# Kernel optimization log

Measured on AMD Instinct MI355X. Metric: run time of the kernel, lower is better.

## Reference

```python
import jax, jax.numpy as jnp
import numpy as np

B, S, H, NH, SLOTS, SD = 4, 2048, 1024, 16, 16, 32
HD = H // NH  # head_dim = 64


def setup_inputs() -> dict:
    key = jax.random.key(0)
    ks = jax.random.split(key, 8)
    def w(k, shape, scale=0.02):
        return jax.random.normal(k, shape, jnp.float32) * scale
    return {
        "hidden_states": jax.random.normal(ks[0], (B, S, H), jnp.float32),
        "stack": jax.random.normal(ks[1], (B, S, NH, SLOTS, SD), jnp.float32),
        "mask": jnp.ones((B, S, NH, SLOTS), jnp.float32),
        "Wa": w(ks[2], (H, 3 * NH)), "ba": jnp.zeros((3 * NH,), jnp.float32),
        "Wd": w(ks[3], (HD, SD)), "bd": jnp.zeros((SD,), jnp.float32),
        "Wu": w(ks[4], (SD, HD)), "bu": jnp.zeros((HD,), jnp.float32),
        "Wg": w(ks[5], (SD, 1)), "bg": jnp.zeros((1,), jnp.float32),
        "res_weight": jnp.ones((1,), jnp.float32),
    }


def reference(hidden_states, stack, mask, Wa, ba, Wd, bd, Wu, bu, Wg, bg, res_weight):
    b, s, h = hidden_states.shape
    # action logits, scaled by sqrt(head_dim), softmax over {push,pop,noop}
    logits = (hidden_states @ Wa + ba) / jnp.sqrt(jnp.float32(HD))
    actions = jax.nn.softmax(logits.reshape(b, s, NH, 3), axis=-1)  # [B,S,NH,3]
    # per-head key values projected down to stack_dim
    k = hidden_states.reshape(b, s, NH, HD) @ Wd + bd  # [B,S,NH,SD]
    # soft push / pop / noop stack update (fused weighted sum; no [.,3,.] stack tensor)
    push_stack = jnp.concatenate([k[..., None, :], stack[..., :-1, :]], axis=3)
    pop_stack = jnp.concatenate([stack[..., 1:, :], jnp.zeros_like(stack[..., :1, :])], axis=3)
    push_mask = jnp.concatenate([jnp.ones_like(mask[..., :1]), mask[..., :-1]], axis=3)
    pop_mask = jnp.concatenate([mask[..., 1:], jnp.zeros_like(mask[..., :1])], axis=3)
    a_push = actions[..., 0]
    a_pop = actions[..., 1]
    a_noop = actions[..., 2]
    new_stack = (a_push[..., None, None] * push_stack
                 + a_pop[..., None, None] * pop_stack
                 + a_noop[..., None, None] * stack)  # [B,S,NH,SLOTS,SD]
    new_mask = (a_push[..., None] * push_mask
                + a_pop[..., None] * pop_mask
                + a_noop[..., None] * mask)  # [B,S,NH,SLOTS]
    # gated readout over stack slots
    gate_scores = (new_stack @ Wg)[..., 0] + bg[0]  # [B,S,NH,SLOTS]
    gate = jax.nn.softmax(gate_scores + (1.0 - new_mask) * -1e9, axis=-1)
    mem = jnp.sum(new_stack * gate[..., None], axis=3)  # [B,S,NH,SD]
    mem = mem @ Wu + bu  # [B,S,NH,HD]
    out = mem.reshape(b, s, h) * res_weight[0] + hidden_states
    return (out, new_stack, new_mask)
```

## Files before the change

### kernel.cpp

```cpp
#include <hip/hip_runtime.h>


constexpr long long OUT_STACK_OFF = 8388608LL;
constexpr long long OUT_MASK_OFF  = 75497472LL;

__global__ void transpose_wa(const float* __restrict__ Wa, float* __restrict__ WaT) {
    int o = blockIdx.x * 256 + threadIdx.x;
    if (o < 48 * 1024) {
        int j = o >> 10, i = o & 1023;
        WaT[o] = Wa[i * 48 + j];
    }
}

__device__ __forceinline__ float dot4(float4 a, float4 b) {
    return a.x * b.x + a.y * b.y + a.z * b.z + a.w * b.w;
}

__device__ __forceinline__ float4 shfl4(float4 v, int src) {
    return make_float4(__shfl(v.x, src), __shfl(v.y, src),
                       __shfl(v.z, src), __shfl(v.w, src));
}

__device__ __forceinline__ float4 sel4(bool c, float4 a, float4 b) {
    return make_float4(c ? a.x : b.x, c ? a.y : b.y, c ? a.z : b.z, c ? a.w : b.w);
}

__global__ __launch_bounds__(256)
void proj_kernel(const float* __restrict__ hid,
                 const float* __restrict__ WaT,
                 const float* __restrict__ ba,
                 const float* __restrict__ Wd,
                 const float* __restrict__ bd,
                 float* __restrict__ out)
{
    const int t = threadIdx.x;
    const int wv = t >> 6, lane = t & 63;
    const int tok0 = blockIdx.x * 4;
    float* stash = out + OUT_STACK_OFF;
    const float4* hid4 = (const float4*)hid + (size_t)tok0 * 256;

    float4 hreg[4][4];
    #pragma unroll
    for (int tt = 0; tt < 4; ++tt)
        #pragma unroll
        for (int m = 0; m < 4; ++m)
            hreg[tt][m] = hid4[tt * 256 + m * 64 + lane];

    const float4* waT4 = (const float4*)WaT;
    #pragma unroll
    for (int jj = 0; jj < 12; ++jj) {
        int j = wv * 12 + jj;
        float a0 = 0.f, a1 = 0.f, a2 = 0.f, a3 = 0.f;
        #pragma unroll
        for (int m = 0; m < 4; ++m) {
            float4 w = waT4[j * 256 + m * 64 + lane];
            a0 += dot4(hreg[0][m], w);
            a1 += dot4(hreg[1][m], w);
            a2 += dot4(hreg[2][m], w);
            a3 += dot4(hreg[3][m], w);
        }
        #pragma unroll
        for (int off = 1; off <= 32; off <<= 1) {
            a0 += __shfl_xor(a0, off);
            a1 += __shfl_xor(a1, off);
            a2 += __shfl_xor(a2, off);
            a3 += __shfl_xor(a3, off);
        }
        if ((lane & 15) == jj) {
            int tt = lane >> 4;
            float v = (tt == 0) ? a0 : (tt == 1) ? a1 : (tt == 2) ? a2 : a3;
            int nh = wv * 4 + jj / 3, a = jj - 3 * (jj / 3);
            stash[(size_t)(tok0 + tt) * 8192 + nh * 512 + 32 + a] = (v + ba[j]) * 0.125f;
        }
    }

    const int d = t & 31, nhg = t >> 5;
    float acc0[4], acc1[4];
    float bdv = bd[d];
    #pragma unroll
    for (int tt = 0; tt < 4; ++tt) { acc0[tt] = bdv; acc1[tt] = bdv; }
    #pragma unroll
    for (int ii = 0; ii < 16; ++ii) {
        float w0 = Wd[(4 * ii + 0) * 32 + d];
        float w1 = Wd[(4 * ii + 1) * 32 + d];
        float w2 = Wd[(4 * ii + 2) * 32 + d];
        float w3 = Wd[(4 * ii + 3) * 32 + d];
        #pragma unroll
        for (int tt = 0; tt < 4; ++tt) {
            float4 ha = hid4[tt * 256 + nhg * 16 + ii];
            float4 hb = hid4[tt * 256 + (nhg + 8) * 16 + ii];
            acc0[tt] += ha.x * w0 + ha.y * w1 + ha.z * w2 + ha.w * w3;
            acc1[tt] += hb.x * w0 + hb.y * w1 + hb.z * w2 + hb.w * w3;
        }
    }
    #pragma unroll
    for (int tt = 0; tt < 4; ++tt) {
        stash[(size_t)(tok0 + tt) * 8192 + nhg * 512 + d] = acc0[tt];
        stash[(size_t)(tok0 + tt) * 8192 + (nhg + 8) * 512 + d] = acc1[tt];
    }
}

__global__ __launch_bounds__(256, 4)
void stack_main(const float* __restrict__ stack,
                const float* __restrict__ mask,
                const float* __restrict__ hid,
                const float* __restrict__ Wg,
                const float* __restrict__ bgp,
                const float* __restrict__ Wu,
                const float* __restrict__ bu,
                const float* __restrict__ resw,
                float* __restrict__ out)
{
    __shared__ __align__(16) float sh_mem[4][32];
    const int t = threadIdx.x, wv = t >> 6, l = t & 63;
    const int wid = blockIdx.x * 4 + wv;
    const int tok = wid >> 4, nh = wid & 15;

    const float4* stk4 = (const float4*)stack + (size_t)tok * 2048 + nh * 128;
    float* ostack = out + OUT_STACK_OFF + (size_t)tok * 8192 + nh * 512;
    const float4* stash4 = (const float4*)ostack;

    float4 A  = stk4[l];
    float4 Bv = stk4[64 + l];
    float4 kv = stash4[l & 7];
    float4 lg = stash4[8];
    const float* mrow_g = mask + (size_t)tok * 256 + nh * 16;
    float mA = mrow_g[l >> 3];
    float mB = mrow_g[8 + (l >> 3)];
    float4 wg = *(const float4*)(Wg + (l & 7) * 4);

    float mx = fmaxf(lg.x, fmaxf(lg.y, lg.z));
    float e0 = __expf(lg.x - mx), e1 = __expf(lg.y - mx), e2 = __expf(lg.z - mx);
    float ainv = 1.f / (e0 + e1 + e2);
    float ap = e0 * ainv, apop = e1 * ainv, an = e2 * ainv;

    float4 Am  = shfl4(A,  l - 8);
    float4 Apl = shfl4(A,  l + 8);
    float4 BfA = shfl4(A,  l + 56);
    float4 AfB = shfl4(Bv, l - 56);
    float4 Bm  = shfl4(Bv, l - 8);
    float4 Bp  = shfl4(Bv, l + 8);
    float sAm = __shfl(mA, l - 8), sAp = __shfl(mA, l + 8), sA56 = __shfl(mA, l + 56);
    float sBm = __shfl(mB, l - 8), sBp = __shfl(mB, l + 8), sB56 = __shfl(mB, l - 56);

    const bool lo = (l < 8), hi = (l >= 56);
    float4 prevA = sel4(lo, kv, Am);
    float4 nextA = sel4(hi, AfB, Apl);
    float4 prevB = sel4(lo, BfA, Bm);
    float4 nextB = sel4(hi, make_float4(0.f, 0.f, 0.f, 0.f), Bp);
    float pmA = lo ? 1.f : sAm;
    float nmA = hi ? sB56 : sAp;
    float pmB = lo ? sA56 : sBm;
    float nmB = hi ? 0.f : sBp;

    float4 nA, nB;
    nA.x = ap * prevA.x + apop * nextA.x + an * A.x;
    nA.y = ap * prevA.y + apop * nextA.y + an * A.y;
    nA.z = ap * prevA.z + apop * nextA.z + an * A.z;
    nA.w = ap * prevA.w + apop * nextA.w + an * A.w;
    nB.x = ap * prevB.x + apop * nextB.x + an * Bv.x;
    nB.y = ap * prevB.y + apop * nextB.y + an * Bv.y;
    nB.z = ap * prevB.z + apop * nextB.z + an * Bv.z;
    nB.w = ap * prevB.w + apop * nextB.w + an * Bv.w;
    float nmaskA = ap * pmA + apop * nmA + an * mA;
    float nmaskB = ap * pmB + apop * nmB + an * mB;

    float4* ost4 = (float4*)ostack;
    ost4[l] = nA;
    ost4[64 + l] = nB;
    if ((l & 7) == 0) {
        float* om = out + OUT_MASK_OFF + (size_t)tok * 256 + nh * 16;
        om[l >> 3] = nmaskA;
        om[8 + (l >> 3)] = nmaskB;
    }

    float gA = dot4(nA, wg);
    float gB = dot4(nB, wg);
    #pragma unroll
    for (int off = 1; off <= 4; off <<= 1) {
        gA += __shfl_xor(gA, off);
        gB += __shfl_xor(gB, off);
    }
    float bgv = bgp[0];
    gA += bgv + (1.f - nmaskA) * -1e9f;
    gB += bgv + (1.f - nmaskB) * -1e9f;

    float gm = fmaxf(gA, gB);
    #pragma unroll
    for (int off = 8; off <= 32; off <<= 1) gm = fmaxf(gm, __shfl_xor(gm, off));
    float eA = __expf(gA - gm), eB = __expf(gB - gm);
    float es = eA + eB;
    #pragma unroll
    for (int off = 8; off <= 32; off <<= 1) es += __shfl_xor(es, off);
    float ginv = 1.f / es;
    float gateA = eA * ginv, gateB = eB * ginv;

    float4 sv;
    sv.x = gateA * nA.x + gateB * nB.x;
    sv.y = gateA * nA.y + gateB * nB.y;
    sv.z = gateA * nA.z + gateB * nB.z;
    sv.w = gateA * nA.w + gateB * nB.w;
    #pragma unroll
    for (int off = 8; off <= 32; off <<= 1) {
        sv.x += __shfl_xor(sv.x, off);
        sv.y += __shfl_xor(sv.y, off);
        sv.z += __shfl_xor(sv.z, off);
        sv.w += __shfl_xor(sv.w, off);
    }
    if (l < 8) *(float4*)&sh_mem[wv][l * 4] = sv;
    __syncthreads();

    float acc = bu[l];
    const float* mrow = sh_mem[wv];
    #pragma unroll
    for (int dd = 0; dd < 32; ++dd)
        acc += mrow[dd] * Wu[dd * 64 + l];
    size_t oidx = (size_t)tok * 1024 + nh * 64 + l;
    out[oidx] = acc * resw[0] + hid[oidx];
}

extern "C" void kernel_launch(void* const* d_in, const int* in_sizes, int n_in,
                              void* d_out, int out_size, void* d_ws, size_t ws_size,
                              hipStream_t stream) {
    const float* hid  = (const float*)d_in[0];
    const float* stk  = (const float*)d_in[1];
    const float* msk  = (const float*)d_in[2];
    const float* Wa   = (const float*)d_in[3];
    const float* ba   = (const float*)d_in[4];
    const float* Wd   = (const float*)d_in[5];
    const float* bd   = (const float*)d_in[6];
    const float* Wu   = (const float*)d_in[7];
    const float* bu   = (const float*)d_in[8];
    const float* Wg   = (const float*)d_in[9];
    const float* bg   = (const float*)d_in[10];
    const float* rw   = (const float*)d_in[11];
    float* out = (float*)d_out;
    float* waT = (float*)d_ws;

    transpose_wa<<<192, 256, 0, stream>>>(Wa, waT);
    proj_kernel<<<2048, 256, 0, stream>>>(hid, waT, ba, Wd, bd, out);
    stack_main<<<32768, 256, 0, stream>>>(stk, msk, hid, Wg, bg, Wu, bu, rw, out);
}
```

Before: 596.7 us.

## Fuse action and key projections into the stack kernel, dropping the stash round-trip

Removes the separate projection kernel and computes the action logits and the down-projected key inside the stack kernel. Each block stages one token's hidden row in shared memory. This avoids writing and re-reading a stash in the output buffer and saves a launch. It also remaps block indices with a swizzle, and the Wu readout now uses shuffles instead of a shared-memory round trip. The cost is that each token's hidden row is loaded by four blocks, and the logit and Wd dot products are now computed per head by each wave instead of being amortised across four tokens.

```diff
diff --git a/kernel.cpp b/kernel.cpp
--- a/kernel.cpp
+++ b/kernel.cpp
@@ -25,85 +25,14 @@
     return make_float4(c ? a.x : b.x, c ? a.y : b.y, c ? a.z : b.z, c ? a.w : b.w);
 }
 
-__global__ __launch_bounds__(256)
-void proj_kernel(const float* __restrict__ hid,
-                 const float* __restrict__ WaT,
-                 const float* __restrict__ ba,
-                 const float* __restrict__ Wd,
-                 const float* __restrict__ bd,
-                 float* __restrict__ out)
-{
-    const int t = threadIdx.x;
-    const int wv = t >> 6, lane = t & 63;
-    const int tok0 = blockIdx.x * 4;
-    float* stash = out + OUT_STACK_OFF;
-    const float4* hid4 = (const float4*)hid + (size_t)tok0 * 256;
-
-    float4 hreg[4][4];
-    #pragma unroll
-    for (int tt = 0; tt < 4; ++tt)
-        #pragma unroll
-        for (int m = 0; m < 4; ++m)
-            hreg[tt][m] = hid4[tt * 256 + m * 64 + lane];
-
-    const float4* waT4 = (const float4*)WaT;
-    #pragma unroll
-    for (int jj = 0; jj < 12; ++jj) {
-        int j = wv * 12 + jj;
-        float a0 = 0.f, a1 = 0.f, a2 = 0.f, a3 = 0.f;
-        #pragma unroll
-        for (int m = 0; m < 4; ++m) {
-            float4 w = waT4[j * 256 + m * 64 + lane];
-            a0 += dot4(hreg[0][m], w);
-            a1 += dot4(hreg[1][m], w);
-            a2 += dot4(hreg[2][m], w);
-            a3 += dot4(hreg[3][m], w);
-        }
-        #pragma unroll
-        for (int off = 1; off <= 32; off <<= 1) {
-            a0 += __shfl_xor(a0, off);
-            a1 += __shfl_xor(a1, off);
-            a2 += __shfl_xor(a2, off);
-            a3 += __shfl_xor(a3, off);
-        }
-        if ((lane & 15) == jj) {
-            int tt = lane >> 4;
-            float v = (tt == 0) ? a0 : (tt == 1) ? a1 : (tt == 2) ? a2 : a3;
-            int nh = wv * 4 + jj / 3, a = jj - 3 * (jj / 3);
-            stash[(size_t)(tok0 + tt) * 8192 + nh * 512 + 32 + a] = (v + ba[j]) * 0.125f;
-        }
-    }
-
-    const int d = t & 31, nhg = t >> 5;
-    float acc0[4], acc1[4];
-    float bdv = bd[d];
-    #pragma unroll
-    for (int tt = 0; tt < 4; ++tt) { acc0[tt] = bdv; acc1[tt] = bdv; }
-    #pragma unroll
-    for (int ii = 0; ii < 16; ++ii) {
-        float w0 = Wd[(4 * ii + 0) * 32 + d];
-        float w1 = Wd[(4 * ii + 1) * 32 + d];
-        float w2 = Wd[(4 * ii + 2) * 32 + d];
-        float w3 = Wd[(4 * ii + 3) * 32 + d];
-        #pragma unroll
-        for (int tt = 0; tt < 4; ++tt) {
-            float4 ha = hid4[tt * 256 + nhg * 16 + ii];
-            float4 hb = hid4[tt * 256 + (nhg + 8) * 16 + ii];
-            acc0[tt] += ha.x * w0 + ha.y * w1 + ha.z * w2 + ha.w * w3;
-            acc1[tt] += hb.x * w0 + hb.y * w1 + hb.z * w2 + hb.w * w3;
-        }
-    }
-    #pragma unroll
-    for (int tt = 0; tt < 4; ++tt) {
-        stash[(size_t)(tok0 + tt) * 8192 + nhg * 512 + d] = acc0[tt];
-        stash[(size_t)(tok0 + tt) * 8192 + (nhg + 8) * 512 + d] = acc1[tt];
-    }
-}
-
 __global__ __launch_bounds__(256, 4)
-void stack_main(const float* __restrict__ stack,
+void stack_main(const float* __restrict__ hid,
+                const float* __restrict__ stack,
                 const float* __restrict__ mask,
-                const float* __restrict__ hid,
+                const float* __restrict__ WaT,
+                const float* __restrict__ ba,
+                const float* __restrict__ Wd,
+                const float* __restrict__ bd,
                 const float* __restrict__ Wg,
                 const float* __restrict__ bgp,
                 const float* __restrict__ Wu,
@@ -111,28 +40,60 @@
                 const float* __restrict__ resw,
                 float* __restrict__ out)
 {
-    __shared__ __align__(16) float sh_mem[4][32];
+    __shared__ __align__(16) float sh_hid[1024];
+
     const int t = threadIdx.x, wv = t >> 6, l = t & 63;
-    const int wid = blockIdx.x * 4 + wv;
-    const int tok = wid >> 4, nh = wid & 15;
+    const int raw = blockIdx.x;
+    const int sb  = (raw >> 3) + ((raw & 7) << 12);
+    const int tok = sb >> 2;
+    const int nh  = ((sb & 3) << 2) + wv;
+
+    const float4* hid4g = (const float4*)(hid + (size_t)tok * 1024);
+    ((float4*)sh_hid)[t] = hid4g[t];
+    __syncthreads();
+
+    float4 hreg[4];
+    #pragma unroll
+    for (int m = 0; m < 4; ++m) hreg[m] = ((const float4*)sh_hid)[m * 64 + l];
+    const float4* waT4 = (const float4*)WaT;
+    float lac[3];
+    #pragma unroll
+    for (int a = 0; a < 3; ++a) {
+        int j = nh * 3 + a;
+        float acc = 0.f;
+        #pragma unroll
+        for (int m = 0; m < 4; ++m)
+            acc += dot4(hreg[m], waT4[j * 256 + m * 64 + l]);
+        #pragma unroll
+        for (int off = 1; off <= 32; off <<= 1) acc += __shfl_xor(acc, off);
+        lac[a] = (acc + ba[j]) * 0.125f;
+    }
+    float mx = fmaxf(lac[0], fmaxf(lac[1], lac[2]));
+    float e0 = __expf(lac[0] - mx), e1 = __expf(lac[1] - mx), e2 = __expf(lac[2] - mx);
+    float ainv = 1.f / (e0 + e1 + e2);
+    float ap = e0 * ainv, apop = e1 * ainv, an = e2 * ainv;
+
+    const int d = l & 31, hh = l >> 5;
+    const float* hrow = sh_hid + nh * 64 + hh * 32;
+    float kacc = 0.f;
+    #pragma unroll
+    for (int i = 0; i < 32; ++i)
+        kacc += hrow[i] * Wd[(hh * 32 + i) * 32 + d];
+    kacc += __shfl_xor(kacc, 32);
+    kacc += bd[d];
+    float4 kv;
+    kv.x = __shfl(kacc, ((l & 7) << 2) + 0);
+    kv.y = __shfl(kacc, ((l & 7) << 2) + 1);
+    kv.z = __shfl(kacc, ((l & 7) << 2) + 2);
+    kv.w = __shfl(kacc, ((l & 7) << 2) + 3);
 
     const float4* stk4 = (const float4*)stack + (size_t)tok * 2048 + nh * 128;
-    float* ostack = out + OUT_STACK_OFF + (size_t)tok * 8192 + nh * 512;
-    const float4* stash4 = (const float4*)ostack;
-
     float4 A  = stk4[l];
     float4 Bv = stk4[64 + l];
-    float4 kv = stash4[l & 7];
-    float4 lg = stash4[8];
     const float* mrow_g = mask + (size_t)tok * 256 + nh * 16;
     float mA = mrow_g[l >> 3];
     float mB = mrow_g[8 + (l >> 3)];
     float4 wg = *(const float4*)(Wg + (l & 7) * 4);
-
-    float mx = fmaxf(lg.x, fmaxf(lg.y, lg.z));
-    float e0 = __expf(lg.x - mx), e1 = __expf(lg.y - mx), e2 = __expf(lg.z - mx);
-    float ainv = 1.f / (e0 + e1 + e2);
-    float ap = e0 * ainv, apop = e1 * ainv, an = e2 * ainv;
 
     float4 Am  = shfl4(A,  l - 8);
     float4 Apl = shfl4(A,  l + 8);
@@ -165,6 +126,7 @@
     float nmaskA = ap * pmA + apop * nmA + an * mA;
     float nmaskB = ap * pmB + apop * nmB + an * mB;
 
+    float* ostack = out + OUT_STACK_OFF + (size_t)tok * 8192 + nh * 512;
     float4* ost4 = (float4*)ostack;
     ost4[l] = nA;
     ost4[64 + l] = nB;
@@ -207,16 +169,18 @@
         sv.z += __shfl_xor(sv.z, off);
         sv.w += __shfl_xor(sv.w, off);
     }
-    if (l < 8) *(float4*)&sh_mem[wv][l * 4] = sv;
-    __syncthreads();
 
     float acc = bu[l];
-    const float* mrow = sh_mem[wv];
-    #pragma unroll
-    for (int dd = 0; dd < 32; ++dd)
-        acc += mrow[dd] * Wu[dd * 64 + l];
+    #pragma unroll
+    for (int q = 0; q < 8; ++q) {
+        float4 mq = shfl4(sv, q);
+        acc += mq.x * Wu[(q * 4 + 0) * 64 + l]
+             + mq.y * Wu[(q * 4 + 1) * 64 + l]
+             + mq.z * Wu[(q * 4 + 2) * 64 + l]
+             + mq.w * Wu[(q * 4 + 3) * 64 + l];
+    }
     size_t oidx = (size_t)tok * 1024 + nh * 64 + l;
-    out[oidx] = acc * resw[0] + hid[oidx];
+    out[oidx] = acc * resw[0] + sh_hid[nh * 64 + l];
 }
 
 extern "C" void kernel_launch(void* const* d_in, const int* in_sizes, int n_in,
@@ -238,6 +202,6 @@
     float* waT = (float*)d_ws;
 
     transpose_wa<<<192, 256, 0, stream>>>(Wa, waT);
-    proj_kernel<<<2048, 256, 0, stream>>>(hid, waT, ba, Wd, bd, out);
-    stack_main<<<32768, 256, 0, stream>>>(stk, msk, hid, Wg, bg, Wu, bu, rw, out);
-}
+    stack_main<<<32768, 256, 0, stream>>>(hid, stk, msk, waT, ba, Wd, bd,
+                                          Wg, bg, Wu, bu, rw, out);
+}
```

Result: slower. 653.0 us (+9.4%).

## Process two heads per wave in stack kernel and use permlane32 swap reductions

Applied to the files above, without the earlier changes.

The stack update kernel now handles two heads per wavefront, which halves the grid and issues the loads for both heads up front so more memory traffic is in flight per wave. The cross-half reduction step (xor 32) in both kernels is replaced with the permlane32_swap builtin when available, avoiding a DPP-unfriendly shuffle. The Wu readout reads the shared memory row as float4. The cost is higher register pressure per thread, which can lower occupancy in a kernel that is mostly bandwidth-bound.

```diff
diff --git a/kernel.cpp b/kernel.cpp
--- a/kernel.cpp
+++ b/kernel.cpp
@@ -24,6 +24,23 @@
 __device__ __forceinline__ float4 sel4(bool c, float4 a, float4 b) {
     return make_float4(c ? a.x : b.x, c ? a.y : b.y, c ? a.z : b.z, c ? a.w : b.w);
 }
+
+#if defined(__has_builtin) && __has_builtin(__builtin_amdgcn_permlane32_swap)
+typedef int v2i_t __attribute__((ext_vector_type(2)));
+__device__ __forceinline__ float red32_add(float x) {
+    v2i_t r = __builtin_amdgcn_permlane32_swap(__float_as_int(x), __float_as_int(x),
+                                               false, false);
+    return __int_as_float(r.x) + __int_as_float(r.y);
+}
+__device__ __forceinline__ float red32_max(float x) {
+    v2i_t r = __builtin_amdgcn_permlane32_swap(__float_as_int(x), __float_as_int(x),
+                                               false, false);
+    return fmaxf(__int_as_float(r.x), __int_as_float(r.y));
+}
+#else
+__device__ __forceinline__ float red32_add(float x) { return x + __shfl_xor(x, 32); }
+__device__ __forceinline__ float red32_max(float x) { return fmaxf(x, __shfl_xor(x, 32)); }
+#endif
 
 __global__ __launch_bounds__(256)
 void proj_kernel(const float* __restrict__ hid,
@@ -60,12 +77,13 @@
             a3 += dot4(hreg[3][m], w);
         }
         #pragma unroll
-        for (int off = 1; off <= 32; off <<= 1) {
+        for (int off = 1; off <= 16; off <<= 1) {
             a0 += __shfl_xor(a0, off);
             a1 += __shfl_xor(a1, off);
             a2 += __shfl_xor(a2, off);
             a3 += __shfl_xor(a3, off);
         }
+        a0 = red32_add(a0); a1 = red32_add(a1); a2 = red32_add(a2); a3 = red32_add(a3);
         if ((lane & 15) == jj) {
             int tt = lane >> 4;
             float v = (tt == 0) ? a0 : (tt == 1) ? a1 : (tt == 2) ? a2 : a3;
@@ -111,112 +129,149 @@
                 const float* __restrict__ resw,
                 float* __restrict__ out)
 {
-    __shared__ __align__(16) float sh_mem[4][32];
+    __shared__ __align__(16) float sh_mem[4][2][32];
     const int t = threadIdx.x, wv = t >> 6, l = t & 63;
-    const int wid = blockIdx.x * 4 + wv;
-    const int tok = wid >> 4, nh = wid & 15;
-
-    const float4* stk4 = (const float4*)stack + (size_t)tok * 2048 + nh * 128;
-    float* ostack = out + OUT_STACK_OFF + (size_t)tok * 8192 + nh * 512;
-    const float4* stash4 = (const float4*)ostack;
-
-    float4 A  = stk4[l];
-    float4 Bv = stk4[64 + l];
-    float4 kv = stash4[l & 7];
-    float4 lg = stash4[8];
-    const float* mrow_g = mask + (size_t)tok * 256 + nh * 16;
-    float mA = mrow_g[l >> 3];
-    float mB = mrow_g[8 + (l >> 3)];
-    float4 wg = *(const float4*)(Wg + (l & 7) * 4);
-
-    float mx = fmaxf(lg.x, fmaxf(lg.y, lg.z));
-    float e0 = __expf(lg.x - mx), e1 = __expf(lg.y - mx), e2 = __expf(lg.z - mx);
-    float ainv = 1.f / (e0 + e1 + e2);
-    float ap = e0 * ainv, apop = e1 * ainv, an = e2 * ainv;
-
-    float4 Am  = shfl4(A,  l - 8);
-    float4 Apl = shfl4(A,  l + 8);
-    float4 BfA = shfl4(A,  l + 56);
-    float4 AfB = shfl4(Bv, l - 56);
-    float4 Bm  = shfl4(Bv, l - 8);
-    float4 Bp  = shfl4(Bv, l + 8);
-    float sAm = __shfl(mA, l - 8), sAp = __shfl(mA, l + 8), sA56 = __shfl(mA, l + 56);
-    float sBm = __shfl(mB, l - 8), sBp = __shfl(mB, l + 8), sB56 = __shfl(mB, l - 56);
-
+    const int bid = blockIdx.x;
+    const int tok = bid >> 1;
+    const int nhb = ((bid & 1) << 3) + wv;
+
+    const float4* stkt = (const float4*)stack + (size_t)tok * 2048;
+    float* ostack_base = out + OUT_STACK_OFF + (size_t)tok * 8192;
+    const float* mrow_g = mask + (size_t)tok * 256;
+
+    float4 A[2], Bv[2], kv[2], lgv[2];
+    float mA[2], mB[2];
+    #pragma unroll
+    for (int u = 0; u < 2; ++u) {
+        const int nh = nhb + 4 * u;
+        const float4* stk4 = stkt + nh * 128;
+        A[u]  = stk4[l];
+        Bv[u] = stk4[64 + l];
+        const float4* stash4 = (const float4*)(ostack_base + nh * 512);
+        kv[u]  = stash4[l & 7];
+        lgv[u] = stash4[8];
+        mA[u] = mrow_g[nh * 16 + (l >> 3)];
+        mB[u] = mrow_g[nh * 16 + 8 + (l >> 3)];
+    }
+    const float4 wg = *(const float4*)(Wg + (l & 7) * 4);
+    const float bgv = bgp[0];
     const bool lo = (l < 8), hi = (l >= 56);
-    float4 prevA = sel4(lo, kv, Am);
-    float4 nextA = sel4(hi, AfB, Apl);
-    float4 prevB = sel4(lo, BfA, Bm);
-    float4 nextB = sel4(hi, make_float4(0.f, 0.f, 0.f, 0.f), Bp);
-    float pmA = lo ? 1.f : sAm;
-    float nmA = hi ? sB56 : sAp;
-    float pmB = lo ? sA56 : sBm;
-    float nmB = hi ? 0.f : sBp;
-
-    float4 nA, nB;
-    nA.x = ap * prevA.x + apop * nextA.x + an * A.x;
-    nA.y = ap * prevA.y + apop * nextA.y + an * A.y;
-    nA.z = ap * prevA.z + apop * nextA.z + an * A.z;
-    nA.w = ap * prevA.w + apop * nextA.w + an * A.w;
-    nB.x = ap * prevB.x + apop * nextB.x + an * Bv.x;
-    nB.y = ap * prevB.y + apop * nextB.y + an * Bv.y;
-    nB.z = ap * prevB.z + apop * nextB.z + an * Bv.z;
-    nB.w = ap * prevB.w + apop * nextB.w + an * Bv.w;
-    float nmaskA = ap * pmA + apop * nmA + an * mA;
-    float nmaskB = ap * pmB + apop * nmB + an * mB;
-
-    float4* ost4 = (float4*)ostack;
-    ost4[l] = nA;
-    ost4[64 + l] = nB;
-    if ((l & 7) == 0) {
-        float* om = out + OUT_MASK_OFF + (size_t)tok * 256 + nh * 16;
-        om[l >> 3] = nmaskA;
-        om[8 + (l >> 3)] = nmaskB;
-    }
-
-    float gA = dot4(nA, wg);
-    float gB = dot4(nB, wg);
-    #pragma unroll
-    for (int off = 1; off <= 4; off <<= 1) {
-        gA += __shfl_xor(gA, off);
-        gB += __shfl_xor(gB, off);
-    }
-    float bgv = bgp[0];
-    gA += bgv + (1.f - nmaskA) * -1e9f;
-    gB += bgv + (1.f - nmaskB) * -1e9f;
-
-    float gm = fmaxf(gA, gB);
-    #pragma unroll
-    for (int off = 8; off <= 32; off <<= 1) gm = fmaxf(gm, __shfl_xor(gm, off));
-    float eA = __expf(gA - gm), eB = __expf(gB - gm);
-    float es = eA + eB;
-    #pragma unroll
-    for (int off = 8; off <= 32; off <<= 1) es += __shfl_xor(es, off);
-    float ginv = 1.f / es;
-    float gateA = eA * ginv, gateB = eB * ginv;
-
-    float4 sv;
-    sv.x = gateA * nA.x + gateB * nB.x;
-    sv.y = gateA * nA.y + gateB * nB.y;
-    sv.z = gateA * nA.z + gateB * nB.z;
-    sv.w = gateA * nA.w + gateB * nB.w;
-    #pragma unroll
-    for (int off = 8; off <= 32; off <<= 1) {
-        sv.x += __shfl_xor(sv.x, off);
-        sv.y += __shfl_xor(sv.y, off);
-        sv.z += __shfl_xor(sv.z, off);
-        sv.w += __shfl_xor(sv.w, off);
-    }
-    if (l < 8) *(float4*)&sh_mem[wv][l * 4] = sv;
+
+    float ap[2], apop[2], an[2];
+    #pragma unroll
+    for (int u = 0; u < 2; ++u) {
+        float mx = fmaxf(lgv[u].x, fmaxf(lgv[u].y, lgv[u].z));
+        float e0 = __expf(lgv[u].x - mx), e1 = __expf(lgv[u].y - mx), e2 = __expf(lgv[u].z - mx);
+        float ainv = 1.f / (e0 + e1 + e2);
+        ap[u] = e0 * ainv; apop[u] = e1 * ainv; an[u] = e2 * ainv;
+    }
+
+    float4 nA[2], nB[2];
+    float nmaskA[2], nmaskB[2];
+    #pragma unroll
+    for (int u = 0; u < 2; ++u) {
+        float4 Am  = shfl4(A[u],  l - 8);
+        float4 Apl = shfl4(A[u],  l + 8);
+        float4 BfA = shfl4(A[u],  l + 56);
+        float4 AfB = shfl4(Bv[u], l - 56);
+        float4 Bm  = shfl4(Bv[u], l - 8);
+        float4 Bp  = shfl4(Bv[u], l + 8);
+        float sAm = __shfl(mA[u], l - 8), sAp = __shfl(mA[u], l + 8), sA56 = __shfl(mA[u], l + 56);
+        float sBm = __shfl(mB[u], l - 8), sBp = __shfl(mB[u], l + 8), sB56 = __shfl(mB[u], l - 56);
+
+        float4 prevA = sel4(lo, kv[u], Am);
+        float4 nextA = sel4(hi, AfB, Apl);
+        float4 prevB = sel4(lo, BfA, Bm);
+        float4 nextB = sel4(hi, make_float4(0.f, 0.f, 0.f, 0.f), Bp);
+        float pmA = lo ? 1.f : sAm;
+        float nmA = hi ? sB56 : sAp;
+        float pmB = lo ? sA56 : sBm;
+        float nmB = hi ? 0.f : sBp;
+
+        nA[u].x = ap[u] * prevA.x + apop[u] * nextA.x + an[u] * A[u].x;
+        nA[u].y = ap[u] * prevA.y + apop[u] * nextA.y + an[u] * A[u].y;
+        nA[u].z = ap[u] * prevA.z + apop[u] * nextA.z + an[u] * A[u].z;
+        nA[u].w = ap[u] * prevA.w + apop[u] * nextA.w + an[u] * A[u].w;
+        nB[u].x = ap[u] * prevB.x + apop[u] * nextB.x + an[u] * Bv[u].x;
+        nB[u].y = ap[u] * prevB.y + apop[u] * nextB.y + an[u] * Bv[u].y;
+        nB[u].z = ap[u] * prevB.z + apop[u] * nextB.z + an[u] * Bv[u].z;
+        nB[u].w = ap[u] * prevB.w + apop[u] * nextB.w + an[u] * Bv[u].w;
+        nmaskA[u] = ap[u] * pmA + apop[u] * nmA + an[u] * mA[u];
+        nmaskB[u] = ap[u] * pmB + apop[u] * nmB + an[u] * mB[u];
+
+        const int nh = nhb + 4 * u;
+        float4* ost4 = (float4*)(ostack_base + nh * 512);
+        ost4[l] = nA[u];
+        ost4[64 + l] = nB[u];
+        if ((l & 7) == 0) {
+            float* om = out + OUT_MASK_OFF + (size_t)tok * 256 + nh * 16;
+            om[l >> 3] = nmaskA[u];
+            om[8 + (l >> 3)] = nmaskB[u];
+        }
+    }
+
+    #pragma unroll
+    for (int u = 0; u < 2; ++u) {
+        float gA = dot4(nA[u], wg);
+        float gB = dot4(nB[u], wg);
+        #pragma unroll
+        for (int off = 1; off <= 4; off <<= 1) {
+            gA += __shfl_xor(gA, off);
+            gB += __shfl_xor(gB, off);
+        }
+        gA += bgv + (1.f - nmaskA[u]) * -1e9f;
+        gB += bgv + (1.f - nmaskB[u]) * -1e9f;
+
+        float gm = fmaxf(gA, gB);
+        gm = fmaxf(gm, __shfl_xor(gm, 8));
+        gm = fmaxf(gm, __shfl_xor(gm, 16));
+        gm = red32_max(gm);
+        float eA = __expf(gA - gm), eB = __expf(gB - gm);
+        float es = eA + eB;
+        es += __shfl_xor(es, 8);
+        es += __shfl_xor(es, 16);
+        es = red32_add(es);
+        float ginv = 1.f / es;
+        float gateA = eA * ginv, gateB = eB * ginv;
+
+        float4 sv;
+        sv.x = gateA * nA[u].x + gateB * nB[u].x;
+        sv.y = gateA * nA[u].y + gateB * nB[u].y;
+        sv.z = gateA * nA[u].z + gateB * nB[u].z;
+        sv.w = gateA * nA[u].w + gateB * nB[u].w;
+        #pragma unroll
+        for (int off = 8; off <= 16; off <<= 1) {
+            sv.x += __shfl_xor(sv.x, off);
+            sv.y += __shfl_xor(sv.y, off);
+            sv.z += __shfl_xor(sv.z, off);
+            sv.w += __shfl_xor(sv.w, off);
+        }
+        sv.x = red32_add(sv.x);
+        sv.y = red32_add(sv.y);
+        sv.z = red32_add(sv.z);
+        sv.w = red32_add(sv.w);
+        if (l < 8) *(float4*)&sh_mem[wv][u][l * 4] = sv;
+    }
     __syncthreads();
 
-    float acc = bu[l];
-    const float* mrow = sh_mem[wv];
-    #pragma unroll
-    for (int dd = 0; dd < 32; ++dd)
-        acc += mrow[dd] * Wu[dd * 64 + l];
-    size_t oidx = (size_t)tok * 1024 + nh * 64 + l;
-    out[oidx] = acc * resw[0] + hid[oidx];
+    const float rw = resw[0];
+    const float buv = bu[l];
+    #pragma unroll
+    for (int u = 0; u < 2; ++u) {
+        float acc = buv;
+        const float4* m4 = (const float4*)sh_mem[wv][u];
+        #pragma unroll
+        for (int q = 0; q < 8; ++q) {
+            float4 mq = m4[q];
+            acc += mq.x * Wu[(q * 4 + 0) * 64 + l]
+                 + mq.y * Wu[(q * 4 + 1) * 64 + l]
+                 + mq.z * Wu[(q * 4 + 2) * 64 + l]
+                 + mq.w * Wu[(q * 4 + 3) * 64 + l];
+        }
+        const int nh = nhb + 4 * u;
+        size_t oidx = (size_t)tok * 1024 + nh * 64 + l;
+        out[oidx] = acc * rw + hid[oidx];
+    }
 }
 
 extern "C" void kernel_launch(void* const* d_in, const int* in_sizes, int n_in,
@@ -239,5 +294,5 @@
 
     transpose_wa<<<192, 256, 0, stream>>>(Wa, waT);
     proj_kernel<<<2048, 256, 0, stream>>>(hid, waT, ba, Wd, bd, out);
-    stack_main<<<32768, 256, 0, stream>>>(stk, msk, hid, Wg, bg, Wu, bu, rw, out);
-}
+    stack_main<<<16384, 256, 0, stream>>>(stk, msk, hid, Wg, bg, Wu, bu, rw, out);
+}
```

New measurement: 601.2 us. No clear change (+0.8%).
